# Kernel tuning notes

Hardware: AMD Instinct MI355X
Metric: run time of the kernel (lower is better)

## Reference

```python
import jax, jax.numpy as jnp
from jax import lax
import numpy as np

LRELU_SLOPE = 0.2
DEMOD_EPS = 1e-8


def _mod_conv(x, style, weight, bias, demodulate, pad):
    """StyleGAN2 modulated conv via grouped conv (groups = batch).
    x: [B,Cin,H,W]; style: [B,Cin]; weight: [Cout,Cin,kh,kw]; bias: [Cout]."""
    B, Cin, H, W = x.shape
    Cout, _, kh, kw = weight.shape
    # per-sample modulated weight [B,Cout,Cin,kh,kw]
    wt = weight[None] * style[:, None, :, None, None]
    if demodulate:
        wt = wt / jnp.sqrt(jnp.sum(wt ** 2, axis=(2, 3, 4), keepdims=True) + DEMOD_EPS)
    out = lax.conv_general_dilated(
        x.reshape(1, B * Cin, H, W),
        wt.reshape(B * Cout, Cin, kh, kw),
        window_strides=(1, 1),
        padding=[(pad, pad), (pad, pad)],
        dimension_numbers=('NCHW', 'OIHW', 'NCHW'),
        feature_group_count=B,
    )
    return out.reshape(B, Cout, H, W) + bias[None, :, None, None]


def setup_inputs() -> dict:
    key = jax.random.key(0)
    ks = jax.random.split(key, 16)
    B, Cin, Cout, Wd, H = 4, 512, 256, 512, 64
    f32 = jnp.float32
    d = {
        'x': jax.random.normal(ks[0], (B, Cin, H, H), f32),
        'w': jax.random.normal(ks[1], (B, Wd), f32),
        # conv1: Cin->Cout 3x3
        'w1': jax.random.normal(ks[2], (Cout, Cin, 3, 3), f32) / np.float32(np.sqrt(Cin * 9)),
        'b1': jax.random.normal(ks[3], (Cout,), f32) * 0.01,
        'a1w': jax.random.normal(ks[4], (Cin, Wd), f32) / np.float32(np.sqrt(Wd)),
        'a1b': jnp.ones((Cin,), f32),
        # conv2: Cout->Cout 3x3
        'w2': jax.random.normal(ks[5], (Cout, Cout, 3, 3), f32) / np.float32(np.sqrt(Cout * 9)),
        'b2': jax.random.normal(ks[6], (Cout,), f32) * 0.01,
        'a2w': jax.random.normal(ks[7], (Cout, Wd), f32) / np.float32(np.sqrt(Wd)),
        'a2b': jnp.ones((Cout,), f32),
        # to_rgb: Cout->3 1x1, no demodulation
        'w3': jax.random.normal(ks[8], (3, Cout, 1, 1), f32) / np.float32(np.sqrt(Cout)),
        'b3': jax.random.normal(ks[9], (3,), f32) * 0.01,
        'a3w': jax.random.normal(ks[10], (Cout, Wd), f32) / np.float32(np.sqrt(Wd)),
        'a3b': jnp.ones((Cout,), f32),
    }
    return d


def reference(x, w, w1, b1, a1w, a1b, w2, b2, a2w, a2b, w3, b3, a3w, a3b):
    B, C, H, W = x.shape
    # nn.Upsample(scale_factor=2, mode='bilinear', align_corners=False) == half-pixel bilinear
    xu = jax.image.resize(x, (B, C, 2 * H, 2 * W), method='bilinear')
    s1 = w @ a1w.T + a1b                      # affine -> per-sample style [B,Cin]
    h = jax.nn.leaky_relu(_mod_conv(xu, s1, w1, b1, True, 1), LRELU_SLOPE)
    s2 = w @ a2w.T + a2b
    h = jax.nn.leaky_relu(_mod_conv(h, s2, w2, b2, True, 1), LRELU_SLOPE)
    s3 = w @ a3w.T + a3b
    rgb = jax.nn.leaky_relu(_mod_conv(h, s3, w3, b3, False, 0), LRELU_SLOPE)
    return (h, rgb)
```

## Files before the change

### kernel.cpp

```cpp
#include <hip/hip_runtime.h>
#include <stdint.h>

typedef __attribute__((ext_vector_type(8))) short bhalf8;
typedef __attribute__((ext_vector_type(4))) float fx4;

__device__ __forceinline__ unsigned short f2bf(float f) {
    unsigned u = __builtin_bit_cast(unsigned, f);
    unsigned r = (u + 0x7fffu + ((u >> 16) & 1u)) >> 16;
    return (unsigned short)r;
}
__device__ __forceinline__ float bf2f(unsigned short h) {
    unsigned u = ((unsigned)h) << 16;
    return __builtin_bit_cast(float, u);
}
__device__ __forceinline__ float lrelu(float v) { return v > 0.f ? v : 0.2f * v; }

typedef __attribute__((address_space(1))) void as1_void;
typedef __attribute__((address_space(3))) void as3_void;
__device__ __forceinline__ void gl_lds16(const void* g, void* l) {
    __builtin_amdgcn_global_load_lds((as1_void*)(void*)g, (as3_void*)l, 16, 0, 0);
}

__global__ __launch_bounds__(256) void style_kernel(
    const float* __restrict__ w,
    const float* __restrict__ a1w, const float* __restrict__ a1b,
    const float* __restrict__ a2w, const float* __restrict__ a2b,
    const float* __restrict__ a3w, const float* __restrict__ a3b,
    float* __restrict__ s1, float* __restrict__ s2, float* __restrict__ s3)
{
    int gw = blockIdx.x * 4 + (threadIdx.x >> 6);
    int lane = threadIdx.x & 63;
    int b = gw >> 10, r = gw & 1023;
    const float* arow; const float* abias; float* dst;
    if (r < 512)      { arow = a1w + (size_t)r * 512;        abias = a1b + r;       dst = s1 + b * 512 + r; }
    else if (r < 768) { int rr = r - 512; arow = a2w + (size_t)rr * 512; abias = a2b + rr; dst = s2 + b * 256 + rr; }
    else              { int rr = r - 768; arow = a3w + (size_t)rr * 512; abias = a3b + rr; dst = s3 + b * 256 + rr; }
    const float* wrow = w + b * 512;
    float acc = 0.f;
    #pragma unroll
    for (int j = 0; j < 8; ++j) {
        int c = lane + j * 64;
        acc += wrow[c] * arow[c];
    }
    #pragma unroll
    for (int off = 32; off; off >>= 1) acc += __shfl_down(acc, off, 64);
    if (lane == 0) *dst = acc + *abias;
}

__global__ __launch_bounds__(256) void demod_kernel(
    const float* __restrict__ w1, const float* __restrict__ w2,
    const float* __restrict__ s1, const float* __restrict__ s2,
    float* __restrict__ d1, float* __restrict__ d2)
{
    int blk = blockIdx.x;
    int conv = blk >> 10, b = (blk >> 8) & 3, o = blk & 255;
    int t = threadIdx.x;
    int cin = conv ? 256 : 512;
    const float* s = conv ? (s2 + b * 256) : (s1 + b * 512);
    const float* row = (conv ? w2 : w1) + (size_t)o * cin * 9;
    __shared__ float sv[512];
    for (int i = t; i < cin; i += 256) { float v = s[i]; sv[i] = v * v; }
    __syncthreads();
    float sum = 0.f;
    int n = cin * 9;
    for (int k = t; k < n; k += 256) {
        float v = row[k];
        sum += v * v * sv[k / 9];
    }
    #pragma unroll
    for (int off = 32; off; off >>= 1) sum += __shfl_down(sum, off, 64);
    __shared__ float red[4];
    if ((t & 63) == 0) red[t >> 6] = sum;
    __syncthreads();
    if (t == 0) {
        float tot = red[0] + red[1] + red[2] + red[3];
        (conv ? d2 : d1)[b * 256 + o] = rsqrtf(tot + 1e-8f);
    }
}

__global__ __launch_bounds__(256) void pack_kernel(
    const float* __restrict__ w1, const float* __restrict__ w2,
    unsigned short* __restrict__ wp1, unsigned short* __restrict__ wp2)
{
    int tid = blockIdx.x * 256 + threadIdx.x;
    const int N1 = 1179648, N2 = 589824;
    if (tid < N1) {
        int e = tid & 7, m = (tid >> 3) & 127, kh = (tid >> 10) & 3;
        int dx = (tid >> 12) % 3, ic = (tid / 12288) & 15;
        int dy = (tid / 196608) % 3, mblk = tid / 589824;
        int o = mblk * 128 + m, ci = ic * 32 + kh * 8 + e;
        wp1[tid] = f2bf(w1[((size_t)o * 512 + ci) * 9 + dy * 3 + dx]);
    } else if (tid < N1 + N2) {
        int t2 = tid - N1;
        int e = t2 & 7, m = (t2 >> 3) & 127, kh = (t2 >> 10) & 3;
        int dx = (t2 >> 12) % 3, ic = (t2 / 12288) & 7;
        int dy = (t2 / 98304) % 3, mblk = t2 / 294912;
        int o = mblk * 128 + m, ci = ic * 32 + kh * 8 + e;
        wp2[t2] = f2bf(w2[((size_t)o * 256 + ci) * 9 + dy * 3 + dx]);
    }
}

__global__ __launch_bounds__(256) void upsample_kernel(
    const float* __restrict__ x, const float* __restrict__ s1,
    unsigned short* __restrict__ xu)
{
    __shared__ float L[2][64][65];
    int bid = blockIdx.x, t = threadIdx.x;
    int yo = bid & 127, b = bid >> 7;
    int k = yo >> 1;
    int sy0, sy1; float wy0, wy1;
    if ((yo & 1) == 0) { sy0 = k > 0 ? k - 1 : 0; sy1 = k; wy0 = 0.25f; wy1 = 0.75f; }
    else               { sy0 = k; sy1 = k < 63 ? k + 1 : 63; wy0 = 0.75f; wy1 = 0.25f; }
    for (int c0 = 0; c0 < 512; c0 += 64) {
        __syncthreads();
        #pragma unroll
        for (int j = 0; j < 32; ++j) {
            int f = t + j * 256;
            int idx = f & 63, rowid = f >> 6;
            int cc = rowid & 63, which = rowid >> 6;
            int sy = which ? sy1 : sy0;
            L[which][cc][idx] = x[((size_t)(b * 512 + c0 + cc) * 64 + sy) * 64 + idx];
        }
        __syncthreads();
        #pragma unroll
        for (int j = 0; j < 16; ++j) {
            int it = t + j * 256;
            int cp = it & 31, xo = it >> 5;
            int kk = xo >> 1, sx0, sx1; float wx0, wx1;
            if ((xo & 1) == 0) { sx0 = kk > 0 ? kk - 1 : 0; sx1 = kk; wx0 = 0.25f; wx1 = 0.75f; }
            else               { sx0 = kk; sx1 = kk < 63 ? kk + 1 : 63; wx0 = 0.75f; wx1 = 0.25f; }
            int c = cp * 2;
            float A0 = wx0 * L[0][c][sx0] + wx1 * L[0][c][sx1];
            float B0 = wx0 * L[1][c][sx0] + wx1 * L[1][c][sx1];
            float A1 = wx0 * L[0][c + 1][sx0] + wx1 * L[0][c + 1][sx1];
            float B1 = wx0 * L[1][c + 1][sx0] + wx1 * L[1][c + 1][sx1];
            float v0 = (wy0 * A0 + wy1 * B0) * s1[b * 512 + c0 + c];
            float v1 = (wy0 * A1 + wy1 * B1) * s1[b * 512 + c0 + c + 1];
            unsigned pk = (unsigned)f2bf(v0) | ((unsigned)f2bf(v1) << 16);
            *(unsigned*)&xu[((size_t)(b * 128 + yo) * 128 + xo) * 512 + c0 + c] = pk;
        }
    }
}

template<int CIN, bool IS_CONV2>
__global__ __launch_bounds__(512, 2) void conv3x3_kernel(
    const unsigned short* __restrict__ inp,
    const unsigned short* __restrict__ wpack,
    const float* __restrict__ dvec,
    const float* __restrict__ bias,
    const float* __restrict__ post,
    unsigned short* __restrict__ outmod,
    float* __restrict__ outf)
{
    constexpr int NIC = CIN / 32;
    __shared__ __attribute__((aligned(16))) short Alds[2][2][12288];
    __shared__ __attribute__((aligned(16))) short Blds[4][4160];
    const int tid = threadIdx.x;
    const int lane = tid & 63;
    const int wvi = tid >> 6;
    const int oh = wvi >> 2;
    const int row = (wvi >> 1) & 1;
    const int wn = (wvi & 1) * 64;
    const int bid = blockIdx.x;
    const int y0 = (bid & 63) << 1;
    const int b = bid >> 6;
    const int lhi = lane >> 4;
    const int llo = lane & 15;

    auto stageA = [&](int bufp, int ic, int dy) {
        const unsigned short* s0 = wpack + ((size_t)(0 + dy) * NIC + ic) * 12288;
        const unsigned short* s1 = wpack + ((size_t)(3 + dy) * NIC + ic) * 12288;
        #pragma unroll
        for (int j = 0; j < 3; ++j) {
            int g = tid + j * 512;
            gl_lds16(s0 + (size_t)g * 8, (char*)&Alds[bufp][0][0] + g * 16);
        }
        #pragma unroll
        for (int j = 0; j < 3; ++j) {
            int g = tid + j * 512;
            gl_lds16(s1 + (size_t)g * 8, (char*)&Alds[bufp][1][0] + g * 16);
        }
    };
    auto stageB = [&](int r, int ic) {
        int yy = y0 - 1 + r;
        char* dst = (char*)&Blds[r][0] + 64 + tid * 16;
        int xg = tid >> 2, i8 = tid & 3;
        int i8s = i8 ^ ((xg >> 1) & 3);
        if ((unsigned)yy < 128u)
            gl_lds16(inp + ((size_t)(b * 128 + yy) * 128 + xg) * CIN + ic * 32 + i8s * 8, dst);
        else
            *(int4*)dst = make_int4(0, 0, 0, 0);
    };

    if (tid < 32) {
        int r = tid >> 3, sl = (tid >> 2) & 1, part = tid & 3;
        *(int4*)((char*)&Blds[r][0] + (sl ? 8256 : 0) + part * 16) = make_int4(0, 0, 0, 0);
    }

    fx4 acc[8][4];
    #pragma unroll
    for (int mt = 0; mt < 8; ++mt)
        #pragma unroll
        for (int nt = 0; nt < 4; ++nt) acc[mt][nt] = (fx4){0.f, 0.f, 0.f, 0.f};

    stageA(0, 0, 0);
    stageB(0, 0);
    stageB(1, 0);
    __syncthreads();

    int buf = 0;
    for (int ic = 0; ic < NIC; ++ic) {
        #pragma unroll
        for (int dy = 0; dy < 3; ++dy) {
            if (dy == 0) {
                stageA(buf ^ 1, ic, 1);
                stageB(2, ic);
            } else if (dy == 1) {
                stageA(buf ^ 1, ic, 2);
                stageB(3, ic);
                if (ic + 1 < NIC) stageB(0, ic + 1);
            } else {
                if (ic + 1 < NIC) { stageA(buf ^ 1, ic + 1, 0); stageB(1, ic + 1); }
            }
            const short* Abase = &Alds[buf][oh][0];
            const short* Brow = &Blds[row + dy][0];
            #pragma unroll
            for (int dx = 0; dx < 3; ++dx) {
                bhalf8 af[8], bfr[4];
                #pragma unroll
                for (int mt = 0; mt < 8; ++mt)
                    af[mt] = *(const bhalf8*)&Abase[dx * 4096 + (lhi * 128 + mt * 16 + llo) * 8];
                #pragma unroll
                for (int nt = 0; nt < 4; ++nt) {
                    int s = wn + nt * 16 + llo + dx;
                    int key = ((s - 1) >> 1) & 3;
                    bfr[nt] = *(const bhalf8*)&Brow[s * 32 + ((lhi ^ key) << 3)];
                }
                #pragma unroll
                for (int mt = 0; mt < 8; ++mt)
                    #pragma unroll
                    for (int nt = 0; nt < 4; ++nt)
                        acc[mt][nt] = __builtin_amdgcn_mfma_f32_16x16x32_bf16(
                            af[mt], bfr[nt], acc[mt][nt], 0, 0, 0);
            }
            __syncthreads();
            buf ^= 1;
        }
    }

    const int y = y0 + row;
    #pragma unroll
    for (int mt = 0; mt < 8; ++mt) {
        const int o0 = oh * 128 + mt * 16 + lhi * 4;
        const fx4 d4 = *(const fx4*)(dvec + b * 256 + o0);
        const fx4 bb4 = *(const fx4*)(bias + o0);
        const fx4 p4 = *(const fx4*)(post + b * 256 + o0);
        #pragma unroll
        for (int nt = 0; nt < 4; ++nt) {
            const int xo = wn + nt * 16 + llo;
            unsigned lo = 0, hi = 0;
            #pragma unroll
            for (int r = 0; r < 4; ++r) {
                float v = acc[mt][nt][r] * d4[r] + bb4[r];
                v = lrelu(v);
                unsigned short ub = f2bf(v * p4[r]);
                if (r < 2) lo |= (unsigned)ub << (16 * r);
                else       hi |= (unsigned)ub << (16 * (r - 2));
            }
            *(uint2*)&outmod[((size_t)(b * 128 + y) * 128 + xo) * 256 + o0] = make_uint2(lo, hi);
        }
    }

    if (IS_CONV2) {
        float* Ef = (float*)&Alds[0][0][0];
        #pragma unroll
        for (int ch = 0; ch < 4; ++ch) {
            const int rc = ch >> 1, ohc = ch & 1;
            __syncthreads();
            if (row == rc && oh == ohc) {
                #pragma unroll
                for (int mt = 0; mt < 8; ++mt) {
                    const int o0 = ohc * 128 + mt * 16 + lhi * 4;
                    const fx4 d4 = *(const fx4*)(dvec + b * 256 + o0);
                    const fx4 bb4 = *(const fx4*)(bias + o0);
                    #pragma unroll
                    for (int nt = 0; nt < 4; ++nt) {
                        const int xo = wn + nt * 16 + llo;
                        #pragma unroll
                        for (int r = 0; r < 4; ++r) {
                            float v = lrelu(acc[mt][nt][r] * d4[r] + bb4[r]);
                            Ef[(mt * 16 + lhi * 4 + r) * 132 + xo] = v;
                        }
                    }
                }
            }
            __syncthreads();
            #pragma unroll
            for (int k = 0; k < 8; ++k) {
                int f = k * 8192 + tid * 16;
                int o_loc = f >> 9, off = f & 511;
                float4 val = *(const float4*)((const char*)Ef + o_loc * 528 + off);
                *(float4*)&outf[(((size_t)b * 256 + ohc * 128 + o_loc) * 128 + (y0 + rc)) * 128 + (off >> 2)] = val;
            }
        }
    }
}

__global__ __launch_bounds__(256) void rgb_kernel(
    const unsigned short* __restrict__ hs3,
    const float* __restrict__ w3, const float* __restrict__ b3,
    float* __restrict__ out)
{
    __shared__ float wl[768];
    int t = threadIdx.x;
    for (int i = t; i < 768; i += 256) wl[i] = w3[i];
    __syncthreads();
    int p = blockIdx.x * 64 + (t >> 2);
    int q = t & 3;
    const unsigned short* src = hs3 + (size_t)p * 256 + q * 64;
    float a0 = 0.f, a1 = 0.f, a2 = 0.f;
    #pragma unroll
    for (int c8 = 0; c8 < 64; c8 += 8) {
        int4 pk = *(const int4*)(src + c8);
        #pragma unroll
        for (int qq = 0; qq < 4; ++qq) {
            unsigned uu = ((const unsigned*)&pk)[qq];
            float ve = bf2f((unsigned short)(uu & 0xffffu));
            float vo = bf2f((unsigned short)(uu >> 16));
            int c = q * 64 + c8 + qq * 2;
            a0 += ve * wl[c] + vo * wl[c + 1];
            a1 += ve * wl[256 + c] + vo * wl[256 + c + 1];
            a2 += ve * wl[512 + c] + vo * wl[512 + c + 1];
        }
    }
    a0 += __shfl_xor(a0, 1, 64); a0 += __shfl_xor(a0, 2, 64);
    a1 += __shfl_xor(a1, 1, 64); a1 += __shfl_xor(a1, 2, 64);
    a2 += __shfl_xor(a2, 1, 64); a2 += __shfl_xor(a2, 2, 64);
    int b = p >> 14, yx = p & 16383;
    if (q < 3) {
        float v = (q == 0) ? a0 : (q == 1) ? a1 : a2;
        out[((size_t)b * 3 + q) * 16384 + yx] = lrelu(v + b3[q]);
    }
}

extern "C" void kernel_launch(void* const* d_in, const int* in_sizes, int n_in,
                              void* d_out, int out_size, void* d_ws, size_t ws_size,
                              hipStream_t stream) {
    const float* x   = (const float*)d_in[0];
    const float* w   = (const float*)d_in[1];
    const float* w1  = (const float*)d_in[2];
    const float* b1  = (const float*)d_in[3];
    const float* a1w = (const float*)d_in[4];
    const float* a1b = (const float*)d_in[5];
    const float* w2  = (const float*)d_in[6];
    const float* b2  = (const float*)d_in[7];
    const float* a2w = (const float*)d_in[8];
    const float* a2b = (const float*)d_in[9];
    const float* w3  = (const float*)d_in[10];
    const float* b3  = (const float*)d_in[11];
    const float* a3w = (const float*)d_in[12];
    const float* a3b = (const float*)d_in[13];

    char* ws = (char*)d_ws;
    unsigned short* xu  = (unsigned short*)(ws);
    unsigned short* hs3 = (unsigned short*)(ws);
    unsigned short* t1  = (unsigned short*)(ws + 67108864);
    unsigned short* wp1 = (unsigned short*)(ws + 100663296);
    unsigned short* wp2 = (unsigned short*)(ws + 103022592);
    float* s1 = (float*)(ws + 104202240);
    float* s2 = (float*)(ws + 104210432);
    float* s3 = (float*)(ws + 104214528);
    float* d1 = (float*)(ws + 104218624);
    float* d2 = (float*)(ws + 104222720);

    float* h_out   = (float*)d_out;
    float* rgb_out = h_out + 16777216;

    style_kernel<<<1024, 256, 0, stream>>>(w, a1w, a1b, a2w, a2b, a3w, a3b, s1, s2, s3);
    demod_kernel<<<2048, 256, 0, stream>>>(w1, w2, s1, s2, d1, d2);
    pack_kernel<<<6912, 256, 0, stream>>>(w1, w2, wp1, wp2);
    upsample_kernel<<<512, 256, 0, stream>>>(x, s1, xu);
    conv3x3_kernel<512, false><<<256, 512, 0, stream>>>(xu, wp1, d1, b1, s2, t1, nullptr);
    conv3x3_kernel<256, true><<<256, 512, 0, stream>>>(t1, wp2, d2, b2, s3, hs3, h_out);
    rgb_kernel<<<1024, 256, 0, stream>>>(hs3, w3, b3, rgb_out);
}
```

Measured before the change: 392.5 us.

## Split conv output channels across blocks: 512 blocks of 256 threads

Each conv block now handles one 128-channel half of the outputs with 4 waves, where it used to cover all 256 channels with 8 waves. This doubles the grid to 512 blocks and halves the shared memory per block, so on a 256-CU device more CUs get work and occupancy can rise. The padded halo columns in the B tile are dropped; the code clamps the column index and zeroes out-of-range fragments in registers instead. In exchange, each input row tile is now loaded twice, once per channel half, which adds global and L2 traffic.

```diff
diff --git a/kernel.cpp b/kernel.cpp
--- a/kernel.cpp
+++ b/kernel.cpp
@@ -143,7 +143,7 @@
 }
 
 template<int CIN, bool IS_CONV2>
-__global__ __launch_bounds__(512, 2) void conv3x3_kernel(
+__global__ __launch_bounds__(256, 2) void conv3x3_kernel(
     const unsigned short* __restrict__ inp,
     const unsigned short* __restrict__ wpack,
     const float* __restrict__ dvec,
@@ -153,50 +153,43 @@
     float* __restrict__ outf)
 {
     constexpr int NIC = CIN / 32;
-    __shared__ __attribute__((aligned(16))) short Alds[2][2][12288];
-    __shared__ __attribute__((aligned(16))) short Blds[4][4160];
+    __shared__ __attribute__((aligned(16))) short Alds[2][12288];
+    __shared__ __attribute__((aligned(16))) short Blds[4][4096];
     const int tid = threadIdx.x;
     const int lane = tid & 63;
     const int wvi = tid >> 6;
-    const int oh = wvi >> 2;
-    const int row = (wvi >> 1) & 1;
+    const int row = wvi >> 1;
     const int wn = (wvi & 1) * 64;
     const int bid = blockIdx.x;
     const int y0 = (bid & 63) << 1;
-    const int b = bid >> 6;
+    const int mblk = (bid >> 6) & 1;
+    const int b = bid >> 7;
     const int lhi = lane >> 4;
     const int llo = lane & 15;
 
     auto stageA = [&](int bufp, int ic, int dy) {
-        const unsigned short* s0 = wpack + ((size_t)(0 + dy) * NIC + ic) * 12288;
-        const unsigned short* s1 = wpack + ((size_t)(3 + dy) * NIC + ic) * 12288;
-        #pragma unroll
-        for (int j = 0; j < 3; ++j) {
-            int g = tid + j * 512;
-            gl_lds16(s0 + (size_t)g * 8, (char*)&Alds[bufp][0][0] + g * 16);
-        }
-        #pragma unroll
-        for (int j = 0; j < 3; ++j) {
-            int g = tid + j * 512;
-            gl_lds16(s1 + (size_t)g * 8, (char*)&Alds[bufp][1][0] + g * 16);
+        const unsigned short* src = wpack + ((size_t)(mblk * 3 + dy) * NIC + ic) * 12288;
+        #pragma unroll
+        for (int j = 0; j < 6; ++j) {
+            int g = tid + j * 256;
+            gl_lds16(src + (size_t)g * 8, (char*)&Alds[bufp][0] + g * 16);
         }
     };
-    auto stageB = [&](int r, int ic) {
+    auto stageB_row = [&](int r, int ic) {
         int yy = y0 - 1 + r;
-        char* dst = (char*)&Blds[r][0] + 64 + tid * 16;
-        int xg = tid >> 2, i8 = tid & 3;
-        int i8s = i8 ^ ((xg >> 1) & 3);
-        if ((unsigned)yy < 128u)
-            gl_lds16(inp + ((size_t)(b * 128 + yy) * 128 + xg) * CIN + ic * 32 + i8s * 8, dst);
-        else
-            *(int4*)dst = make_int4(0, 0, 0, 0);
+        #pragma unroll
+        for (int j = 0; j < 2; ++j) {
+            int g = tid + j * 256;
+            int xg = g >> 2, i8 = g & 3;
+            int i8s = i8 ^ ((xg >> 1) & 3);
+            char* dst = (char*)&Blds[r][0] + g * 16;
+            if ((unsigned)yy < 128u)
+                gl_lds16(inp + ((size_t)(b * 128 + yy) * 128 + xg) * CIN + ic * 32 + i8s * 8, dst);
+            else
+                *(int4*)dst = make_int4(0, 0, 0, 0);
+        }
     };
 
-    if (tid < 32) {
-        int r = tid >> 3, sl = (tid >> 2) & 1, part = tid & 3;
-        *(int4*)((char*)&Blds[r][0] + (sl ? 8256 : 0) + part * 16) = make_int4(0, 0, 0, 0);
-    }
-
     fx4 acc[8][4];
     #pragma unroll
     for (int mt = 0; mt < 8; ++mt)
@@ -204,37 +197,38 @@
         for (int nt = 0; nt < 4; ++nt) acc[mt][nt] = (fx4){0.f, 0.f, 0.f, 0.f};
 
     stageA(0, 0, 0);
-    stageB(0, 0);
-    stageB(1, 0);
+    stageB_row(0, 0);
+    stageB_row(1, 0);
     __syncthreads();
 
-    int buf = 0;
     for (int ic = 0; ic < NIC; ++ic) {
         #pragma unroll
-        for (int dy = 0; dy < 3; ++dy) {
-            if (dy == 0) {
-                stageA(buf ^ 1, ic, 1);
-                stageB(2, ic);
-            } else if (dy == 1) {
-                stageA(buf ^ 1, ic, 2);
-                stageB(3, ic);
-                if (ic + 1 < NIC) stageB(0, ic + 1);
-            } else {
-                if (ic + 1 < NIC) { stageA(buf ^ 1, ic + 1, 0); stageB(1, ic + 1); }
-            }
-            const short* Abase = &Alds[buf][oh][0];
-            const short* Brow = &Blds[row + dy][0];
+        for (int p = 0; p < 3; ++p) {
+            const int buf = (ic + p) & 1;
+            if (p < 2) stageA(buf ^ 1, ic, p + 1);
+            else if (ic + 1 < NIC) stageA(buf ^ 1, ic + 1, 0);
+            if (p == 0) { stageB_row(2, ic); stageB_row(3, ic); }
+            else if (ic + 1 < NIC) {
+                if (p == 1) stageB_row(0, ic + 1);
+                else        stageB_row(1, ic + 1);
+            }
+            const short* Abase = &Alds[buf][0];
+            const short* Brow  = &Blds[row + p][0];
             #pragma unroll
             for (int dx = 0; dx < 3; ++dx) {
                 bhalf8 af[8], bfr[4];
                 #pragma unroll
                 for (int mt = 0; mt < 8; ++mt)
-                    af[mt] = *(const bhalf8*)&Abase[dx * 4096 + (lhi * 128 + mt * 16 + llo) * 8];
+                    af[mt] = *(const bhalf8*)&Abase[dx * 4096 + lhi * 1024 + (mt * 16 + llo) * 8];
                 #pragma unroll
                 for (int nt = 0; nt < 4; ++nt) {
-                    int s = wn + nt * 16 + llo + dx;
-                    int key = ((s - 1) >> 1) & 3;
-                    bfr[nt] = *(const bhalf8*)&Brow[s * 32 + ((lhi ^ key) << 3)];
+                    int x = wn + nt * 16 + llo + dx - 1;
+                    int xs = x < 0 ? 0 : (x > 127 ? 127 : x);
+                    int key = (xs >> 1) & 3;
+                    bfr[nt] = *(const bhalf8*)&Brow[xs * 32 + ((lhi ^ key) << 3)];
+                    if (dx != 1) {
+                        if (x != xs) { bhalf8 z = {0,0,0,0,0,0,0,0}; bfr[nt] = z; }
+                    }
                 }
                 #pragma unroll
                 for (int mt = 0; mt < 8; ++mt)
@@ -244,14 +238,13 @@
                             af[mt], bfr[nt], acc[mt][nt], 0, 0, 0);
             }
             __syncthreads();
-            buf ^= 1;
         }
     }
 
     const int y = y0 + row;
     #pragma unroll
     for (int mt = 0; mt < 8; ++mt) {
-        const int o0 = oh * 128 + mt * 16 + lhi * 4;
+        const int o0 = mblk * 128 + mt * 16 + lhi * 4;
         const fx4 d4 = *(const fx4*)(dvec + b * 256 + o0);
         const fx4 bb4 = *(const fx4*)(bias + o0);
         const fx4 p4 = *(const fx4*)(post + b * 256 + o0);
@@ -272,24 +265,25 @@
     }
 
     if (IS_CONV2) {
-        float* Ef = (float*)&Alds[0][0][0];
+        float* Ef = (float*)&Alds[0][0];
         #pragma unroll
         for (int ch = 0; ch < 4; ++ch) {
-            const int rc = ch >> 1, ohc = ch & 1;
+            const int rc = ch >> 1, oh2 = ch & 1;
             __syncthreads();
-            if (row == rc && oh == ohc) {
+            if (row == rc) {
                 #pragma unroll
-                for (int mt = 0; mt < 8; ++mt) {
-                    const int o0 = ohc * 128 + mt * 16 + lhi * 4;
-                    const fx4 d4 = *(const fx4*)(dvec + b * 256 + o0);
-                    const fx4 bb4 = *(const fx4*)(bias + o0);
+                for (int mi = 0; mi < 4; ++mi) {
+                    const int mt = oh2 * 4 + mi;
+                    const int ol = mblk * 128 + mt * 16 + lhi * 4;
+                    const fx4 d4 = *(const fx4*)(dvec + b * 256 + ol);
+                    const fx4 bb4 = *(const fx4*)(bias + ol);
                     #pragma unroll
                     for (int nt = 0; nt < 4; ++nt) {
                         const int xo = wn + nt * 16 + llo;
                         #pragma unroll
                         for (int r = 0; r < 4; ++r) {
                             float v = lrelu(acc[mt][nt][r] * d4[r] + bb4[r]);
-                            Ef[(mt * 16 + lhi * 4 + r) * 132 + xo] = v;
+                            Ef[(mi * 16 + lhi * 4 + r) * 132 + xo] = v;
                         }
                     }
                 }
@@ -297,10 +291,10 @@
             __syncthreads();
             #pragma unroll
             for (int k = 0; k < 8; ++k) {
-                int f = k * 8192 + tid * 16;
-                int o_loc = f >> 9, off = f & 511;
-                float4 val = *(const float4*)((const char*)Ef + o_loc * 528 + off);
-                *(float4*)&outf[(((size_t)b * 256 + ohc * 128 + o_loc) * 128 + (y0 + rc)) * 128 + (off >> 2)] = val;
+                int f = k * 256 + tid;
+                int o_loc = f >> 5, xq = f & 31;
+                float4 val = *(const float4*)&Ef[o_loc * 132 + xq * 4];
+                *(float4*)&outf[(((size_t)b * 256 + mblk * 128 + oh2 * 64 + o_loc) * 128 + (y0 + rc)) * 128 + xq * 4] = val;
             }
         }
     }
@@ -380,7 +374,7 @@
     demod_kernel<<<2048, 256, 0, stream>>>(w1, w2, s1, s2, d1, d2);
     pack_kernel<<<6912, 256, 0, stream>>>(w1, w2, wp1, wp2);
     upsample_kernel<<<512, 256, 0, stream>>>(x, s1, xu);
-    conv3x3_kernel<512, false><<<256, 512, 0, stream>>>(xu, wp1, d1, b1, s2, t1, nullptr);
-    conv3x3_kernel<256, true><<<256, 512, 0, stream>>>(t1, wp2, d2, b2, s3, hs3, h_out);
+    conv3x3_kernel<512, false><<<512, 256, 0, stream>>>(xu, wp1, d1, b1, s2, t1, nullptr);
+    conv3x3_kernel<256, true><<<512, 256, 0, stream>>>(t1, wp2, d2, b2, s3, hs3, h_out);
     rgb_kernel<<<1024, 256, 0, stream>>>(hs3, w3, b3, rgb_out);
 }
```

After: 386.5 us. About the same (-1.5%).
